# Performance work log

Hardware: AMD Instinct MI355X
Metric: run time of the kernel (lower is better)

The kernel has to match this reference:

```python
import jax, jax.numpy as jnp
import numpy as np

EPS = 1e-10
LEAKY_SLOPE = 0.01


def norm_1(x):
    mx = jnp.max(x)
    mn = jnp.min(x)
    return (x - mn) / (mx - mn + EPS)


def intr(f_cat):
    # channel self-attention: [b,c,h,w] -> attention over channels
    b, c, h, w = f_cat.shape
    fr = f_cat.reshape(b, c, h * w)                      # [b,c,n]
    scores = jnp.einsum('bcn,bdn->bcd', fr, fr)          # [b,c,c]
    W = jax.nn.softmax(scores, axis=1)                   # softmax over dim 1 (rows)
    fw = jnp.einsum('bcd,bdn->bcn', W, fr).reshape(b, c, h, w)
    return norm_1(jnp.maximum(f_cat - jnp.mean(f_cat), EPS)) + fw + f_cat


def conv3x3(x, w, b):
    y = jax.lax.conv_general_dilated(
        x, w, window_strides=(1, 1), padding='SAME',
        dimension_numbers=('NCHW', 'OIHW', 'NCHW'))
    return y + b[None, :, None, None]


def setup_inputs() -> dict:
    key = jax.random.key(0)
    ks = jax.random.split(key, 13)
    shp = (4, 64, 128, 128)
    names = ['E1_0', 'E1_1', 'E2_0', 'E2_1', 'E3_0', 'E3_1', 'E4_0', 'E4_1']
    d = {n: jax.random.normal(k, shp, dtype=jnp.float32)
         for n, k in zip(names, ks[:8])}
    d['fc'] = jax.random.normal(ks[8], (4, 128, 128, 128), dtype=jnp.float32)
    d['conv1_w'] = jax.random.normal(ks[9], (64, 128, 3, 3), dtype=jnp.float32) * 0.05
    d['conv1_b'] = jax.random.normal(ks[10], (64,), dtype=jnp.float32) * 0.05
    d['conv2_w'] = jax.random.normal(ks[11], (1, 64, 3, 3), dtype=jnp.float32) * 0.05
    d['conv2_b'] = jax.random.normal(ks[12], (1,), dtype=jnp.float32) * 0.05
    return d


def reference(E1_0, E1_1, E2_0, E2_1, E3_0, E3_1, E4_0, E4_1, fc,
              conv1_w, conv1_b, conv2_w, conv2_b):
    cat_features = jax.nn.leaky_relu(conv3x3(fc, conv1_w, conv1_b), LEAKY_SLOPE)
    activation_maps = conv3x3(cat_features, conv2_w, conv2_b)
    nam = norm_1(activation_maps)
    Ir_activation = nam
    Vi_activation = 1.0 - nam

    M1 = jnp.concatenate([intr(E1_0), intr(E2_0), intr(E3_0), intr(E4_0)], axis=1)
    M2 = jnp.concatenate([intr(E1_1), intr(E2_1), intr(E3_1), intr(E4_1)], axis=1)

    Ir_map = Ir_activation * cat_features
    Vi_map = Vi_activation * cat_features
    b = E4_0.shape[0]
    return (M1, M2,
            M1.reshape(b, -1), M2.reshape(b, -1),
            Ir_map.reshape(Ir_map.shape[0], -1), Vi_map.reshape(Vi_map.shape[0], -1),
            Ir_activation, Vi_activation)
```

## Files before the change

kernel.cpp:

```cpp
#include <hip/hip_runtime.h>
#include <stdint.h>
#include <math.h>

typedef float f4 __attribute__((ext_vector_type(4)));
typedef float f32x4 __attribute__((ext_vector_type(4)));
typedef short bf16x8 __attribute__((ext_vector_type(8)));
typedef _Float16 f16x8 __attribute__((ext_vector_type(8)));
typedef unsigned short u16;
typedef unsigned short u16x4 __attribute__((ext_vector_type(4)));

#define NPIX 16384

#define O_M1   0l
#define O_M2   16777216l
#define O_M1F  33554432l
#define O_M2F  50331648l
#define O_IR   67108864l
#define O_VI   71303168l
#define O_IRA  75497472l
#define O_VIA  75563008l
#define FLATD  33554432l

#define WS_SUMP 0
#define WS_MMXE 4096
#define WS_MMXA 4160
#define WS_MEAN 4224
#define WS_MNT  4256
#define WS_INV  4288
#define WS_W1M  8192
#define WS_AM   262144
#define WS_WB   524288

struct EPtrs { const float* p[8]; };

__device__ __forceinline__ u16 f2bf(float x){
  unsigned u = __float_as_uint(x);
  unsigned r = (u + 0x7fffu + ((u >> 16) & 1u)) >> 16;
  return (u16)r;
}
__device__ __forceinline__ float bf2f(u16 v){
  return __uint_as_float(((unsigned)v) << 16);
}
__device__ __forceinline__ u16 f2h(float x){
  _Float16 h = (_Float16)x;
  u16 r; __builtin_memcpy(&r, &h, 2);
  return r;
}
__device__ __forceinline__ unsigned fenc(float x){
  unsigned u = __float_as_uint(x);
  return (u & 0x80000000u) ? ~u : (u | 0x80000000u);
}
__device__ __forceinline__ float fdec(unsigned u){
  unsigned v = (u & 0x80000000u) ? (u & 0x7fffffffu) : ~u;
  return __uint_as_float(v);
}

__global__ void k_prep(const float* __restrict__ w1, u16* __restrict__ w1m,
                       unsigned* mmxe, unsigned* mmxa){
  if (blockIdx.x == 0 && threadIdx.x < 9){
    int t = threadIdx.x;
    if (t < 8){ mmxe[2*t] = 0xFFFFFFFFu; mmxe[2*t+1] = 0u; }
    else      { mmxa[0] = 0xFFFFFFFFu; mmxa[1] = 0u; }
  }
  int i = blockIdx.x*256 + threadIdx.x;
  if (i < 73728){
    int ic32 = i & 31;
    int oc   = (i >> 5) & 63;
    int k9   = (i >> 11) % 9;
    int icc  = i / 18432;
    float v = w1[(oc*128 + icc*32 + ic32)*9 + k9];
    w1m[i] = f2h(v);
  }
}

__global__ __launch_bounds__(256) void k_stats_gram(EPtrs eps,
    float* __restrict__ gram, float* __restrict__ sump, unsigned* __restrict__ mmxe){
  int bid = blockIdx.x;
  int t = bid >> 7; int rb = bid & 127; int b = rb >> 5; int s = rb & 31;
  const float* E = eps.p[t];
  __shared__ u16 lds[64*136];
  __shared__ float red[768];
  int tid = threadIdx.x;
  int lane = tid & 63, wave = tid >> 6;
  f32x4 acc[4];
  #pragma unroll
  for (int i=0;i<4;++i) acc[i] = (f32x4){0.f,0.f,0.f,0.f};
  float vmin = 3.4e38f, vmax = -3.4e38f, vsum = 0.f;
  int rowS = tid >> 5;
  int colS = (tid & 31) * 4;
  int rA = wave*16 + (lane & 15);
  int kb = (lane >> 4) * 8;
  long nbase = (long)s * 512;
  for (int ch = 0; ch < 4; ++ch){
    long n0 = nbase + ch*128;
    __syncthreads();
    #pragma unroll
    for (int p = 0; p < 8; ++p){
      int row = p*8 + rowS;
      f4 v = *(const f4*)&E[(long)(b*64 + row)*NPIX + n0 + colS];
      vsum += v[0]+v[1]+v[2]+v[3];
      vmin = fminf(vmin, fminf(fminf(v[0],v[1]), fminf(v[2],v[3])));
      vmax = fmaxf(vmax, fmaxf(fmaxf(v[0],v[1]), fmaxf(v[2],v[3])));
      u16x4 w; w[0]=f2bf(v[0]); w[1]=f2bf(v[1]); w[2]=f2bf(v[2]); w[3]=f2bf(v[3]);
      *(u16x4*)&lds[row*136 + colS] = w;
    }
    __syncthreads();
    #pragma unroll
    for (int ks = 0; ks < 4; ++ks){
      bf16x8 a = *(bf16x8*)&lds[rA*136 + ks*32 + kb];
      #pragma unroll
      for (int cb = 0; cb < 4; ++cb){
        bf16x8 bb = *(bf16x8*)&lds[(cb*16 + (lane&15))*136 + ks*32 + kb];
        acc[cb] = __builtin_amdgcn_mfma_f32_16x16x32_bf16(a, bb, acc[cb], 0, 0, 0);
      }
    }
  }
  long gbase = ((long)((t*4 + b)*32 + s)) * 4096;
  #pragma unroll
  for (int cb = 0; cb < 4; ++cb){
    int d = cb*16 + (lane & 15);
    #pragma unroll
    for (int rr = 0; rr < 4; ++rr){
      int c = 16*wave + 4*(lane>>4) + rr;
      gram[gbase + c*64 + d] = acc[cb][rr];
    }
  }
  red[tid] = vsum; red[256+tid] = vmin; red[512+tid] = vmax;
  __syncthreads();
  for (int off = 128; off > 0; off >>= 1){
    if (tid < off){
      red[tid] += red[tid+off];
      red[256+tid] = fminf(red[256+tid], red[256+tid+off]);
      red[512+tid] = fmaxf(red[512+tid], red[512+tid+off]);
    }
    __syncthreads();
  }
  if (tid == 0){
    sump[t*128 + b*32 + s] = red[0];
    atomicMin(&mmxe[2*t], fenc(red[256]));
    atomicMax(&mmxe[2*t+1], fenc(red[512]));
  }
}

__global__ __launch_bounds__(1024) void k_softmax(const float* __restrict__ gram,
                          u16* __restrict__ Wb,
                          const float* __restrict__ sump, const unsigned* __restrict__ mmxe,
                          float* __restrict__ meanA, float* __restrict__ mntA, float* __restrict__ invA){
  int bid = blockIdx.x; int t = bid >> 2; int b = bid & 3;
  __shared__ float S[64*68];
  int tid = threadIdx.x;
  if (b == 0 && tid == 0){
    float s = 0.f;
    for (int j = 0; j < 128; ++j) s += sump[t*128 + j];
    float mean = s / 4194304.0f;
    float mn = fdec(mmxe[2*t]), mx = fdec(mmxe[2*t+1]);
    float mnt = fmaxf(mn - mean, 1e-10f);
    float mxt = fmaxf(mx - mean, 1e-10f);
    meanA[t] = mean; mntA[t] = mnt;
    invA[t] = 1.0f / (mxt - mnt + 1e-10f);
  }
  long gb = (long)(t*4 + b)*32*4096;
  {
    int i = tid;
    f4 a = (f4){0.f,0.f,0.f,0.f};
    #pragma unroll
    for (int s = 0; s < 32; ++s) a += *(const f4*)&gram[gb + s*4096 + i*4];
    int c = i >> 4, d0 = (i & 15)*4;
    *(f4*)&S[c*68 + d0] = a;
  }
  __syncthreads();
  if (tid < 64){
    int d = tid;
    float mx = -3.4e38f;
    for (int c = 0; c < 64; ++c) mx = fmaxf(mx, S[c*68+d]);
    float sum = 0.f;
    for (int c = 0; c < 64; ++c){ float e = expf(S[c*68+d]-mx); S[c*68+d] = e; sum += e; }
    float inv = 1.0f/sum;
    long wb = (long)(t*4 + b)*4096;
    for (int c = 0; c < 64; ++c) Wb[wb + c*64 + d] = f2bf(S[c*68+d]*inv);
  }
}

__global__ __launch_bounds__(512) void k_conv1(const float* __restrict__ fc,
    const u16* __restrict__ w1m, const float* __restrict__ b1, float* __restrict__ cat){
  int bid = blockIdx.x;
  int vb = (bid & 7)*64 + (bid >> 3);
  int b = vb >> 7, h = vb & 127;
  __shared__ u16 xin[32*3*140];
  int tid = threadIdx.x;
  int lane = tid & 63, wv = tid >> 6;
  int mg = wv >> 2, ng = wv & 3;
  int l15 = lane & 15, lq = lane >> 4;
  if (tid < 192){
    int ic = tid / 6, rem = tid % 6;
    int r = rem >> 1, sx = (rem & 1) ? 132 : 3;
    xin[(ic*3 + r)*140 + sx] = 0;
  }
  f32x4 acc[2][2];
  #pragma unroll
  for (int i=0;i<2;++i)
    #pragma unroll
    for (int j=0;j<2;++j) acc[i][j] = (f32x4){0.f,0.f,0.f,0.f};
  for (int icc = 0; icc < 4; ++icc){
    __syncthreads();
    #pragma unroll
    for (int it = 0; it < 6; ++it){
      int idx = tid + it*512;
      int ic = idx / 96, rem = idx % 96;
      int r = rem >> 5, q = rem & 31;
      int hr = h + r - 1;
      f4 v = (f4){0.f,0.f,0.f,0.f};
      if ((unsigned)hr < 128u)
        v = *(const f4*)&fc[(long)((b*128 + icc*32 + ic)*128 + hr)*128 + 4*q];
      u16x4 w; w[0]=f2h(v[0]); w[1]=f2h(v[1]); w[2]=f2h(v[2]); w[3]=f2h(v[3]);
      *(u16x4*)&xin[(ic*3 + r)*140 + 4 + 4*q] = w;
    }
    __syncthreads();
    #pragma unroll
    for (int kh = 0; kh < 3; ++kh){
      #pragma unroll
      for (int kw = 0; kw < 3; ++kw){
        int k9 = kh*3 + kw;
        f16x8 A[2];
        #pragma unroll
        for (int mi = 0; mi < 2; ++mi){
          int m = mg*2 + mi;
          A[mi] = *(const f16x8*)&w1m[(((icc*9 + k9)*64) + m*16 + l15)*32 + lq*8];
        }
        #pragma unroll
        for (int ji = 0; ji < 2; ++ji){
          int s = ng*32 + ji*16 + l15 + kw + 3;
          int kb = lq*8;
          f16x8 bv;
          #pragma unroll
          for (int e = 0; e < 8; ++e){
            u16 raw = xin[((kb + e)*3 + kh)*140 + s];
            _Float16 hh; __builtin_memcpy(&hh, &raw, 2);
            bv[e] = hh;
          }
          acc[0][ji] = __builtin_amdgcn_mfma_f32_16x16x32_f16(A[0], bv, acc[0][ji], 0, 0, 0);
          acc[1][ji] = __builtin_amdgcn_mfma_f32_16x16x32_f16(A[1], bv, acc[1][ji], 0, 0, 0);
        }
      }
    }
  }
  #pragma unroll
  for (int mi = 0; mi < 2; ++mi){
    #pragma unroll
    for (int rr = 0; rr < 4; ++rr){
      int oc = (mg*2 + mi)*16 + lq*4 + rr;
      float bb = b1[oc];
      #pragma unroll
      for (int ji = 0; ji < 2; ++ji){
        int w = ng*32 + ji*16 + l15;
        float v = acc[mi][ji][rr] + bb;
        v = v > 0.f ? v : 0.01f*v;
        cat[(long)((b*64 + oc)*128 + h)*128 + w] = v;
      }
    }
  }
}

__global__ __launch_bounds__(256) void k_conv2(const float* __restrict__ cat,
    const float* __restrict__ w2, const float* __restrict__ b2p,
    float* __restrict__ am, unsigned* __restrict__ mmxa){
  int bid = blockIdx.x; int b = bid >> 7; int h = bid & 127;
  __shared__ u16 l2[64*3*136];
  __shared__ float w2l[576];
  __shared__ float red2[256];
  int tid = threadIdx.x;
  for (int i = tid; i < 576; i += 256) w2l[i] = w2[i];
  if (tid < 192){
    int ic = tid / 3, r = tid % 3;
    l2[ic*408 + r*136 + 3]   = 0;
    l2[ic*408 + r*136 + 132] = 0;
  }
  #pragma unroll
  for (int rep = 0; rep < 3; ++rep){
    int idx = rep*256 + tid;
    int ic = idx / 12; int rem = idx - ic*12; int r = rem >> 2; int q = rem & 3;
    int hr = h + r - 1;
    #pragma unroll
    for (int k = 0; k < 8; ++k){
      int w = q*32 + 4*k;
      f4 v = (f4){0.f,0.f,0.f,0.f};
      if ((unsigned)hr < 128u)
        v = *(const f4*)&cat[(long)((b*64 + ic)*128 + hr)*128 + w];
      u16x4 u; u[0]=f2bf(v[0]); u[1]=f2bf(v[1]); u[2]=f2bf(v[2]); u[3]=f2bf(v[3]);
      *(u16x4*)&l2[ic*408 + r*136 + 4 + w] = u;
    }
  }
  __syncthreads();
  int w = tid & 127, icg = tid >> 7;
  float a = 0.f;
  for (int ic = icg*32; ic < icg*32+32; ++ic){
    #pragma unroll
    for (int r = 0; r < 3; ++r)
      #pragma unroll
      for (int kw = 0; kw < 3; ++kw)
        a = fmaf(bf2f(l2[ic*408 + r*136 + (w + kw + 3)]), w2l[ic*9 + r*3 + kw], a);
  }
  red2[tid] = a;
  __syncthreads();
  float av = 0.f;
  if (icg == 0){
    av = red2[w] + red2[128 + w] + b2p[0];
    am[(long)(b*128 + h)*128 + w] = av;
  }
  __syncthreads();
  red2[tid] = (icg == 0) ? av : -3.4e38f;
  __syncthreads();
  for (int off = 128; off > 0; off >>= 1){
    if (tid < off) red2[tid] = fmaxf(red2[tid], red2[tid+off]);
    __syncthreads();
  }
  if (tid == 0) atomicMax(&mmxa[1], fenc(red2[0]));
  __syncthreads();
  red2[tid] = (icg == 0) ? av : 3.4e38f;
  __syncthreads();
  for (int off = 128; off > 0; off >>= 1){
    if (tid < off) red2[tid] = fminf(red2[tid], red2[tid+off]);
    __syncthreads();
  }
  if (tid == 0) atomicMin(&mmxa[0], fenc(red2[0]));
}

__global__ void k_maps(const float* __restrict__ am,
                       const unsigned* __restrict__ mmxa, float* __restrict__ out){
  int bid = blockIdx.x;
  int tid = threadIdx.x;
  float mn = fdec(mmxa[0]);
  float inv = 1.0f / (fdec(mmxa[1]) - mn + 1e-10f);
  long e = ((long)bid*256 + tid) * 4;
  f4 c = *(const f4*)&out[O_IR + e];
  f4 a = *(const f4*)&am[(e >> 20)*16384 + (e & 16383)];
  f4 nam = (a - mn) * inv;
  f4 ir = nam * c;
  f4 vi = (1.0f - nam) * c;
  __builtin_nontemporal_store(ir, (f4*)&out[O_IR + e]);
  __builtin_nontemporal_store(vi, (f4*)&out[O_VI + e]);
  if (tid < 4){
    long e2 = ((long)bid*4 + tid) * 4;
    f4 a2 = *(const f4*)&am[e2];
    f4 nam2 = (a2 - mn) * inv;
    f4 via = 1.0f - nam2;
    __builtin_nontemporal_store(nam2, (f4*)&out[O_IRA + e2]);
    __builtin_nontemporal_store(via,  (f4*)&out[O_VIA + e2]);
  }
}

__global__ __launch_bounds__(256, 4) void k_fuse(EPtrs eps, const u16* __restrict__ Wb,
    const float* __restrict__ meanA, const float* __restrict__ mntA, const float* __restrict__ invA,
    float* __restrict__ out){
  int bid = blockIdx.x;
  int t = bid >> 9; int rem = bid & 511; int b = rem >> 7; int nt = rem & 127;
  const float* E = eps.p[t];
  const u16* Wp = Wb + (long)(t*4 + b)*4096;
  __shared__ float tileF[8192];
  int tid = threadIdx.x; int lane = tid & 63; int w = tid >> 6;
  int jc = lane & 15, lq = lane >> 4;
  long n0 = (long)nt * 128;
  long eb = (long)(b*64) * NPIX;
  bf16x8 Wf[2][4];
  #pragma unroll
  for (int ks = 0; ks < 2; ++ks)
    #pragma unroll
    for (int ci = 0; ci < 4; ++ci)
      Wf[ks][ci] = *(const bf16x8*)&Wp[(ci*16 + jc)*64 + ks*32 + lq*8];
  #pragma unroll
  for (int it = 0; it < 8; ++it){
    int a = it*4 + w;
    int c0 = (a >> 1) << 2;
    int n = (a & 1)*64 + lane;
    long src = eb + (long)c0*NPIX + n0 + n;
    float f0 = E[src];
    float f1 = E[src + NPIX];
    float f2 = E[src + 2*NPIX];
    float f3 = E[src + 3*NPIX];
    f32x4 v = {f0, f1, f2, f3};
    *(f32x4*)&tileF[n*64 + (((c0 >> 2) ^ (n & 15)) << 2)] = v;
  }
  __syncthreads();
  f32x4 acc[2][4];
  #pragma unroll
  for (int i=0;i<2;++i)
    #pragma unroll
    for (int j=0;j<4;++j) acc[i][j] = (f32x4){0.f,0.f,0.f,0.f};
  int nw = w*32;
  #pragma unroll
  for (int ks = 0; ks < 2; ++ks){
    #pragma unroll
    for (int j = 0; j < 2; ++j){
      int n_t = nw + j*16 + jc;
      int p = ks*8 + lq*2;
      const float* base = &tileF[n_t*64];
      f32x4 q0 = *(const f32x4*)&base[(p ^ jc) << 2];
      f32x4 q1 = *(const f32x4*)&base[((p+1) ^ jc) << 2];
      bf16x8 av;
      av[0]=(short)f2bf(q0[0]); av[1]=(short)f2bf(q0[1]);
      av[2]=(short)f2bf(q0[2]); av[3]=(short)f2bf(q0[3]);
      av[4]=(short)f2bf(q1[0]); av[5]=(short)f2bf(q1[1]);
      av[6]=(short)f2bf(q1[2]); av[7]=(short)f2bf(q1[3]);
      #pragma unroll
      for (int ci = 0; ci < 4; ++ci)
        acc[j][ci] = __builtin_amdgcn_mfma_f32_16x16x32_bf16(av, Wf[ks][ci], acc[j][ci], 0, 0, 0);
    }
  }
  float mean = meanA[t], mnt = mntA[t], inv = invA[t];
  long Mbase = (t & 1) ? O_M2 : O_M1;
  long gr = t >> 1;
  #pragma unroll
  for (int j = 0; j < 2; ++j){
    int nbase2 = nw + j*16 + lq*4;
    #pragma unroll
    for (int ci = 0; ci < 4; ++ci){
      int c = ci*16 + jc;
      f4 vals;
      #pragma unroll
      for (int rr = 0; rr < 4; ++rr){
        int n_t = nbase2 + rr;
        float f = tileF[n_t*64 + ((((c >> 2) ^ (n_t & 15)) << 2) + (c & 3))];
        float tv = fmaxf(f - mean, 1e-10f);
        vals[rr] = (tv - mnt)*inv + acc[j][ci][rr] + f;
      }
      long dst = Mbase + ((long)(b*256 + gr*64 + c))*NPIX + n0 + nbase2;
      __builtin_nontemporal_store(vals, (f4*)&out[dst]);
      __builtin_nontemporal_store(vals, (f4*)&out[dst + FLATD]);
    }
  }
}

extern "C" void kernel_launch(void* const* d_in, const int* in_sizes, int n_in,
                              void* d_out, int out_size, void* d_ws, size_t ws_size,
                              hipStream_t stream){
  (void)in_sizes; (void)n_in; (void)out_size; (void)ws_size;
  EPtrs ep;
  for (int i = 0; i < 8; ++i) ep.p[i] = (const float*)d_in[i];
  const float* fc = (const float*)d_in[8];
  const float* w1 = (const float*)d_in[9];
  const float* b1 = (const float*)d_in[10];
  const float* w2 = (const float*)d_in[11];
  const float* b2 = (const float*)d_in[12];
  float* out = (float*)d_out;
  char* ws = (char*)d_ws;
  float* sump   = (float*)(ws + WS_SUMP);
  unsigned* mmxe = (unsigned*)(ws + WS_MMXE);
  unsigned* mmxa = (unsigned*)(ws + WS_MMXA);
  float* meanA  = (float*)(ws + WS_MEAN);
  float* mntA   = (float*)(ws + WS_MNT);
  float* invA   = (float*)(ws + WS_INV);
  u16*   w1m    = (u16*)(ws + WS_W1M);
  float* am     = (float*)(ws + WS_AM);
  u16*   Wb     = (u16*)(ws + WS_WB);
  float* gram = out + O_M1F;
  float* cat  = out + O_IR;

  k_prep      <<<288, 256, 0, stream>>>(w1, w1m, mmxe, mmxa);
  k_conv1     <<<512, 512, 0, stream>>>(fc, w1m, b1, cat);
  k_conv2     <<<512, 256, 0, stream>>>(cat, w2, b2, am, mmxa);
  k_maps      <<<4096,256, 0, stream>>>(am, mmxa, out);
  k_stats_gram<<<1024,256, 0, stream>>>(ep, gram, sump, mmxe);
  k_softmax   <<<32, 1024, 0, stream>>>(gram, Wb, sump, mmxe, meanA, mntA, invA);
  k_fuse      <<<4096,256, 0, stream>>>(ep, Wb, meanA, mntA, invA, out);
}
```

Baseline: 201.1 us.

## Merge independent stages into combined kernels to run stats/gram alongside conv

Independent work is packed into shared launches. Stats+gram and conv1 now run in one kernel, dispatched by block index. Conv2 and softmax share a second kernel, which uses a shared-memory union. Conv1 drops from 512 threads to 256 per block, with each wave covering 64 columns instead of 32. The aim is to cut launch gaps and let the memory-bound gram blocks overlap with the compute-bound conv blocks, at the cost of higher register use in conv1 and fewer threads for the softmax gram reduction.

```diff
diff --git a/kernel.cpp b/kernel.cpp
--- a/kernel.cpp
+++ b/kernel.cpp
@@ -73,256 +73,257 @@
   }
 }
 
-__global__ __launch_bounds__(256) void k_stats_gram(EPtrs eps,
-    float* __restrict__ gram, float* __restrict__ sump, unsigned* __restrict__ mmxe){
+struct SGsh { u16 lds[64*136]; float red[768]; };
+struct C1sh { u16 xin[32*3*140]; };
+union  KAsh { SGsh sg; C1sh c1; };
+
+__global__ __launch_bounds__(256) void k_A(EPtrs eps,
+    const float* __restrict__ fc, const u16* __restrict__ w1m, const float* __restrict__ b1,
+    float* __restrict__ gram, float* __restrict__ sump, unsigned* __restrict__ mmxe,
+    float* __restrict__ cat){
+  __shared__ KAsh sh;
   int bid = blockIdx.x;
-  int t = bid >> 7; int rb = bid & 127; int b = rb >> 5; int s = rb & 31;
-  const float* E = eps.p[t];
-  __shared__ u16 lds[64*136];
-  __shared__ float red[768];
   int tid = threadIdx.x;
   int lane = tid & 63, wave = tid >> 6;
-  f32x4 acc[4];
-  #pragma unroll
-  for (int i=0;i<4;++i) acc[i] = (f32x4){0.f,0.f,0.f,0.f};
-  float vmin = 3.4e38f, vmax = -3.4e38f, vsum = 0.f;
-  int rowS = tid >> 5;
-  int colS = (tid & 31) * 4;
-  int rA = wave*16 + (lane & 15);
-  int kb = (lane >> 4) * 8;
-  long nbase = (long)s * 512;
-  for (int ch = 0; ch < 4; ++ch){
-    long n0 = nbase + ch*128;
-    __syncthreads();
-    #pragma unroll
-    for (int p = 0; p < 8; ++p){
-      int row = p*8 + rowS;
-      f4 v = *(const f4*)&E[(long)(b*64 + row)*NPIX + n0 + colS];
-      vsum += v[0]+v[1]+v[2]+v[3];
-      vmin = fminf(vmin, fminf(fminf(v[0],v[1]), fminf(v[2],v[3])));
-      vmax = fmaxf(vmax, fmaxf(fmaxf(v[0],v[1]), fmaxf(v[2],v[3])));
-      u16x4 w; w[0]=f2bf(v[0]); w[1]=f2bf(v[1]); w[2]=f2bf(v[2]); w[3]=f2bf(v[3]);
-      *(u16x4*)&lds[row*136 + colS] = w;
-    }
-    __syncthreads();
-    #pragma unroll
-    for (int ks = 0; ks < 4; ++ks){
-      bf16x8 a = *(bf16x8*)&lds[rA*136 + ks*32 + kb];
-      #pragma unroll
-      for (int cb = 0; cb < 4; ++cb){
-        bf16x8 bb = *(bf16x8*)&lds[(cb*16 + (lane&15))*136 + ks*32 + kb];
-        acc[cb] = __builtin_amdgcn_mfma_f32_16x16x32_bf16(a, bb, acc[cb], 0, 0, 0);
-      }
-    }
-  }
-  long gbase = ((long)((t*4 + b)*32 + s)) * 4096;
-  #pragma unroll
-  for (int cb = 0; cb < 4; ++cb){
-    int d = cb*16 + (lane & 15);
-    #pragma unroll
-    for (int rr = 0; rr < 4; ++rr){
-      int c = 16*wave + 4*(lane>>4) + rr;
-      gram[gbase + c*64 + d] = acc[cb][rr];
-    }
-  }
-  red[tid] = vsum; red[256+tid] = vmin; red[512+tid] = vmax;
-  __syncthreads();
-  for (int off = 128; off > 0; off >>= 1){
-    if (tid < off){
-      red[tid] += red[tid+off];
-      red[256+tid] = fminf(red[256+tid], red[256+tid+off]);
-      red[512+tid] = fmaxf(red[512+tid], red[512+tid+off]);
-    }
-    __syncthreads();
-  }
-  if (tid == 0){
-    sump[t*128 + b*32 + s] = red[0];
-    atomicMin(&mmxe[2*t], fenc(red[256]));
-    atomicMax(&mmxe[2*t+1], fenc(red[512]));
-  }
-}
-
-__global__ __launch_bounds__(1024) void k_softmax(const float* __restrict__ gram,
-                          u16* __restrict__ Wb,
-                          const float* __restrict__ sump, const unsigned* __restrict__ mmxe,
-                          float* __restrict__ meanA, float* __restrict__ mntA, float* __restrict__ invA){
-  int bid = blockIdx.x; int t = bid >> 2; int b = bid & 3;
-  __shared__ float S[64*68];
+  if (bid < 1024){
+    int t = bid >> 7; int rb = bid & 127; int b = rb >> 5; int s = rb & 31;
+    const float* E = eps.p[t];
+    f32x4 acc[4];
+    #pragma unroll
+    for (int i=0;i<4;++i) acc[i] = (f32x4){0.f,0.f,0.f,0.f};
+    float vmin = 3.4e38f, vmax = -3.4e38f, vsum = 0.f;
+    int rowS = tid >> 5;
+    int colS = (tid & 31) * 4;
+    int rA = wave*16 + (lane & 15);
+    int kb = (lane >> 4) * 8;
+    long nbase = (long)s * 512;
+    for (int ch = 0; ch < 4; ++ch){
+      long n0 = nbase + ch*128;
+      __syncthreads();
+      #pragma unroll
+      for (int p = 0; p < 8; ++p){
+        int row = p*8 + rowS;
+        f4 v = *(const f4*)&E[(long)(b*64 + row)*NPIX + n0 + colS];
+        vsum += v[0]+v[1]+v[2]+v[3];
+        vmin = fminf(vmin, fminf(fminf(v[0],v[1]), fminf(v[2],v[3])));
+        vmax = fmaxf(vmax, fmaxf(fmaxf(v[0],v[1]), fmaxf(v[2],v[3])));
+        u16x4 w; w[0]=f2bf(v[0]); w[1]=f2bf(v[1]); w[2]=f2bf(v[2]); w[3]=f2bf(v[3]);
+        *(u16x4*)&sh.sg.lds[row*136 + colS] = w;
+      }
+      __syncthreads();
+      #pragma unroll
+      for (int ks = 0; ks < 4; ++ks){
+        bf16x8 a = *(bf16x8*)&sh.sg.lds[rA*136 + ks*32 + kb];
+        #pragma unroll
+        for (int cb = 0; cb < 4; ++cb){
+          bf16x8 bb = *(bf16x8*)&sh.sg.lds[(cb*16 + (lane&15))*136 + ks*32 + kb];
+          acc[cb] = __builtin_amdgcn_mfma_f32_16x16x32_bf16(a, bb, acc[cb], 0, 0, 0);
+        }
+      }
+    }
+    long gbase = ((long)((t*4 + b)*32 + s)) * 4096;
+    #pragma unroll
+    for (int cb = 0; cb < 4; ++cb){
+      int d = cb*16 + (lane & 15);
+      #pragma unroll
+      for (int rr = 0; rr < 4; ++rr){
+        int c = 16*wave + 4*(lane>>4) + rr;
+        gram[gbase + c*64 + d] = acc[cb][rr];
+      }
+    }
+    sh.sg.red[tid] = vsum; sh.sg.red[256+tid] = vmin; sh.sg.red[512+tid] = vmax;
+    __syncthreads();
+    for (int off = 128; off > 0; off >>= 1){
+      if (tid < off){
+        sh.sg.red[tid] += sh.sg.red[tid+off];
+        sh.sg.red[256+tid] = fminf(sh.sg.red[256+tid], sh.sg.red[256+tid+off]);
+        sh.sg.red[512+tid] = fmaxf(sh.sg.red[512+tid], sh.sg.red[512+tid+off]);
+      }
+      __syncthreads();
+    }
+    if (tid == 0){
+      sump[t*128 + b*32 + s] = sh.sg.red[0];
+      atomicMin(&mmxe[2*t], fenc(sh.sg.red[256]));
+      atomicMax(&mmxe[2*t+1], fenc(sh.sg.red[512]));
+    }
+  } else {
+    int cb = bid - 1024;
+    int vb = (cb & 7)*64 + (cb >> 3);
+    int b = vb >> 7, h = vb & 127;
+    int mg = wave >> 1, ng = wave & 1;
+    int l15 = lane & 15, lq = lane >> 4;
+    if (tid < 192){
+      int ic = tid / 6, rem = tid % 6;
+      int r = rem >> 1, sx = (rem & 1) ? 132 : 3;
+      sh.c1.xin[(ic*3 + r)*140 + sx] = 0;
+    }
+    f32x4 acc[2][4];
+    #pragma unroll
+    for (int i=0;i<2;++i)
+      #pragma unroll
+      for (int j=0;j<4;++j) acc[i][j] = (f32x4){0.f,0.f,0.f,0.f};
+    for (int icc = 0; icc < 4; ++icc){
+      __syncthreads();
+      #pragma unroll
+      for (int it = 0; it < 12; ++it){
+        int idx = it*256 + tid;
+        int ic = idx / 96, rem = idx % 96;
+        int r = rem >> 5, q = rem & 31;
+        int hr = h + r - 1;
+        f4 v = (f4){0.f,0.f,0.f,0.f};
+        if ((unsigned)hr < 128u)
+          v = *(const f4*)&fc[(long)((b*128 + icc*32 + ic)*128 + hr)*128 + 4*q];
+        u16x4 w; w[0]=f2h(v[0]); w[1]=f2h(v[1]); w[2]=f2h(v[2]); w[3]=f2h(v[3]);
+        *(u16x4*)&sh.c1.xin[(ic*3 + r)*140 + 4 + 4*q] = w;
+      }
+      __syncthreads();
+      #pragma unroll
+      for (int kh = 0; kh < 3; ++kh){
+        #pragma unroll
+        for (int kw = 0; kw < 3; ++kw){
+          int k9 = kh*3 + kw;
+          f16x8 A[2];
+          #pragma unroll
+          for (int mi = 0; mi < 2; ++mi){
+            int m = mg*2 + mi;
+            A[mi] = *(const f16x8*)&w1m[(((icc*9 + k9)*64) + m*16 + l15)*32 + lq*8];
+          }
+          #pragma unroll
+          for (int ji = 0; ji < 4; ++ji){
+            int s = ng*64 + ji*16 + l15 + kw + 3;
+            int kb = lq*8;
+            f16x8 bv;
+            #pragma unroll
+            for (int e = 0; e < 8; ++e){
+              u16 raw = sh.c1.xin[((kb + e)*3 + kh)*140 + s];
+              _Float16 hh; __builtin_memcpy(&hh, &raw, 2);
+              bv[e] = hh;
+            }
+            acc[0][ji] = __builtin_amdgcn_mfma_f32_16x16x32_f16(A[0], bv, acc[0][ji], 0, 0, 0);
+            acc[1][ji] = __builtin_amdgcn_mfma_f32_16x16x32_f16(A[1], bv, acc[1][ji], 0, 0, 0);
+          }
+        }
+      }
+    }
+    #pragma unroll
+    for (int mi = 0; mi < 2; ++mi){
+      #pragma unroll
+      for (int rr = 0; rr < 4; ++rr){
+        int oc = (mg*2 + mi)*16 + lq*4 + rr;
+        float bb = b1[oc];
+        #pragma unroll
+        for (int ji = 0; ji < 4; ++ji){
+          int w = ng*64 + ji*16 + l15;
+          float v = acc[mi][ji][rr] + bb;
+          v = v > 0.f ? v : 0.01f*v;
+          cat[(long)((b*64 + oc)*128 + h)*128 + w] = v;
+        }
+      }
+    }
+  }
+}
+
+struct C2sh { u16 l2[64*3*136]; float w2l[576]; float red2[256]; };
+struct SMsh { float S[64*68]; };
+union  KBsh { C2sh c2; SMsh sm; };
+
+__global__ __launch_bounds__(256) void k_B(const float* __restrict__ gram,
+    u16* __restrict__ Wb, const float* __restrict__ sump, const unsigned* __restrict__ mmxe,
+    float* __restrict__ meanA, float* __restrict__ mntA, float* __restrict__ invA,
+    const float* __restrict__ cat, const float* __restrict__ w2, const float* __restrict__ b2p,
+    float* __restrict__ am, unsigned* __restrict__ mmxa){
+  __shared__ KBsh sh;
+  int bid = blockIdx.x;
   int tid = threadIdx.x;
-  if (b == 0 && tid == 0){
-    float s = 0.f;
-    for (int j = 0; j < 128; ++j) s += sump[t*128 + j];
-    float mean = s / 4194304.0f;
-    float mn = fdec(mmxe[2*t]), mx = fdec(mmxe[2*t+1]);
-    float mnt = fmaxf(mn - mean, 1e-10f);
-    float mxt = fmaxf(mx - mean, 1e-10f);
-    meanA[t] = mean; mntA[t] = mnt;
-    invA[t] = 1.0f / (mxt - mnt + 1e-10f);
-  }
-  long gb = (long)(t*4 + b)*32*4096;
-  {
-    int i = tid;
-    f4 a = (f4){0.f,0.f,0.f,0.f};
-    #pragma unroll
-    for (int s = 0; s < 32; ++s) a += *(const f4*)&gram[gb + s*4096 + i*4];
-    int c = i >> 4, d0 = (i & 15)*4;
-    *(f4*)&S[c*68 + d0] = a;
-  }
-  __syncthreads();
-  if (tid < 64){
-    int d = tid;
-    float mx = -3.4e38f;
-    for (int c = 0; c < 64; ++c) mx = fmaxf(mx, S[c*68+d]);
-    float sum = 0.f;
-    for (int c = 0; c < 64; ++c){ float e = expf(S[c*68+d]-mx); S[c*68+d] = e; sum += e; }
-    float inv = 1.0f/sum;
-    long wb = (long)(t*4 + b)*4096;
-    for (int c = 0; c < 64; ++c) Wb[wb + c*64 + d] = f2bf(S[c*68+d]*inv);
-  }
-}
-
-__global__ __launch_bounds__(512) void k_conv1(const float* __restrict__ fc,
-    const u16* __restrict__ w1m, const float* __restrict__ b1, float* __restrict__ cat){
-  int bid = blockIdx.x;
-  int vb = (bid & 7)*64 + (bid >> 3);
-  int b = vb >> 7, h = vb & 127;
-  __shared__ u16 xin[32*3*140];
-  int tid = threadIdx.x;
-  int lane = tid & 63, wv = tid >> 6;
-  int mg = wv >> 2, ng = wv & 3;
-  int l15 = lane & 15, lq = lane >> 4;
-  if (tid < 192){
-    int ic = tid / 6, rem = tid % 6;
-    int r = rem >> 1, sx = (rem & 1) ? 132 : 3;
-    xin[(ic*3 + r)*140 + sx] = 0;
-  }
-  f32x4 acc[2][2];
-  #pragma unroll
-  for (int i=0;i<2;++i)
-    #pragma unroll
-    for (int j=0;j<2;++j) acc[i][j] = (f32x4){0.f,0.f,0.f,0.f};
-  for (int icc = 0; icc < 4; ++icc){
-    __syncthreads();
-    #pragma unroll
-    for (int it = 0; it < 6; ++it){
-      int idx = tid + it*512;
-      int ic = idx / 96, rem = idx % 96;
-      int r = rem >> 5, q = rem & 31;
+  if (bid < 512){
+    int b = bid >> 7; int h = bid & 127;
+    for (int i = tid; i < 576; i += 256) sh.c2.w2l[i] = w2[i];
+    if (tid < 192){
+      int ic = tid / 3, r = tid % 3;
+      sh.c2.l2[ic*408 + r*136 + 3]   = 0;
+      sh.c2.l2[ic*408 + r*136 + 132] = 0;
+    }
+    #pragma unroll
+    for (int rep = 0; rep < 3; ++rep){
+      int idx = rep*256 + tid;
+      int ic = idx / 12; int rem = idx - ic*12; int r = rem >> 2; int q = rem & 3;
       int hr = h + r - 1;
-      f4 v = (f4){0.f,0.f,0.f,0.f};
-      if ((unsigned)hr < 128u)
-        v = *(const f4*)&fc[(long)((b*128 + icc*32 + ic)*128 + hr)*128 + 4*q];
-      u16x4 w; w[0]=f2h(v[0]); w[1]=f2h(v[1]); w[2]=f2h(v[2]); w[3]=f2h(v[3]);
-      *(u16x4*)&xin[(ic*3 + r)*140 + 4 + 4*q] = w;
-    }
-    __syncthreads();
-    #pragma unroll
-    for (int kh = 0; kh < 3; ++kh){
-      #pragma unroll
-      for (int kw = 0; kw < 3; ++kw){
-        int k9 = kh*3 + kw;
-        f16x8 A[2];
+      #pragma unroll
+      for (int k = 0; k < 8; ++k){
+        int w = q*32 + 4*k;
+        f4 v = (f4){0.f,0.f,0.f,0.f};
+        if ((unsigned)hr < 128u)
+          v = *(const f4*)&cat[(long)((b*64 + ic)*128 + hr)*128 + w];
+        u16x4 u; u[0]=f2bf(v[0]); u[1]=f2bf(v[1]); u[2]=f2bf(v[2]); u[3]=f2bf(v[3]);
+        *(u16x4*)&sh.c2.l2[ic*408 + r*136 + 4 + w] = u;
+      }
+    }
+    __syncthreads();
+    int w = tid & 127, icg = tid >> 7;
+    float a = 0.f;
+    for (int ic = icg*32; ic < icg*32+32; ++ic){
+      #pragma unroll
+      for (int r = 0; r < 3; ++r)
         #pragma unroll
-        for (int mi = 0; mi < 2; ++mi){
-          int m = mg*2 + mi;
-          A[mi] = *(const f16x8*)&w1m[(((icc*9 + k9)*64) + m*16 + l15)*32 + lq*8];
-        }
-        #pragma unroll
-        for (int ji = 0; ji < 2; ++ji){
-          int s = ng*32 + ji*16 + l15 + kw + 3;
-          int kb = lq*8;
-          f16x8 bv;
-          #pragma unroll
-          for (int e = 0; e < 8; ++e){
-            u16 raw = xin[((kb + e)*3 + kh)*140 + s];
-            _Float16 hh; __builtin_memcpy(&hh, &raw, 2);
-            bv[e] = hh;
-          }
-          acc[0][ji] = __builtin_amdgcn_mfma_f32_16x16x32_f16(A[0], bv, acc[0][ji], 0, 0, 0);
-          acc[1][ji] = __builtin_amdgcn_mfma_f32_16x16x32_f16(A[1], bv, acc[1][ji], 0, 0, 0);
-        }
-      }
-    }
-  }
-  #pragma unroll
-  for (int mi = 0; mi < 2; ++mi){
-    #pragma unroll
-    for (int rr = 0; rr < 4; ++rr){
-      int oc = (mg*2 + mi)*16 + lq*4 + rr;
-      float bb = b1[oc];
-      #pragma unroll
-      for (int ji = 0; ji < 2; ++ji){
-        int w = ng*32 + ji*16 + l15;
-        float v = acc[mi][ji][rr] + bb;
-        v = v > 0.f ? v : 0.01f*v;
-        cat[(long)((b*64 + oc)*128 + h)*128 + w] = v;
-      }
-    }
-  }
-}
-
-__global__ __launch_bounds__(256) void k_conv2(const float* __restrict__ cat,
-    const float* __restrict__ w2, const float* __restrict__ b2p,
-    float* __restrict__ am, unsigned* __restrict__ mmxa){
-  int bid = blockIdx.x; int b = bid >> 7; int h = bid & 127;
-  __shared__ u16 l2[64*3*136];
-  __shared__ float w2l[576];
-  __shared__ float red2[256];
-  int tid = threadIdx.x;
-  for (int i = tid; i < 576; i += 256) w2l[i] = w2[i];
-  if (tid < 192){
-    int ic = tid / 3, r = tid % 3;
-    l2[ic*408 + r*136 + 3]   = 0;
-    l2[ic*408 + r*136 + 132] = 0;
-  }
-  #pragma unroll
-  for (int rep = 0; rep < 3; ++rep){
-    int idx = rep*256 + tid;
-    int ic = idx / 12; int rem = idx - ic*12; int r = rem >> 2; int q = rem & 3;
-    int hr = h + r - 1;
-    #pragma unroll
-    for (int k = 0; k < 8; ++k){
-      int w = q*32 + 4*k;
-      f4 v = (f4){0.f,0.f,0.f,0.f};
-      if ((unsigned)hr < 128u)
-        v = *(const f4*)&cat[(long)((b*64 + ic)*128 + hr)*128 + w];
-      u16x4 u; u[0]=f2bf(v[0]); u[1]=f2bf(v[1]); u[2]=f2bf(v[2]); u[3]=f2bf(v[3]);
-      *(u16x4*)&l2[ic*408 + r*136 + 4 + w] = u;
-    }
-  }
-  __syncthreads();
-  int w = tid & 127, icg = tid >> 7;
-  float a = 0.f;
-  for (int ic = icg*32; ic < icg*32+32; ++ic){
-    #pragma unroll
-    for (int r = 0; r < 3; ++r)
-      #pragma unroll
-      for (int kw = 0; kw < 3; ++kw)
-        a = fmaf(bf2f(l2[ic*408 + r*136 + (w + kw + 3)]), w2l[ic*9 + r*3 + kw], a);
-  }
-  red2[tid] = a;
-  __syncthreads();
-  float av = 0.f;
-  if (icg == 0){
-    av = red2[w] + red2[128 + w] + b2p[0];
-    am[(long)(b*128 + h)*128 + w] = av;
-  }
-  __syncthreads();
-  red2[tid] = (icg == 0) ? av : -3.4e38f;
-  __syncthreads();
-  for (int off = 128; off > 0; off >>= 1){
-    if (tid < off) red2[tid] = fmaxf(red2[tid], red2[tid+off]);
-    __syncthreads();
-  }
-  if (tid == 0) atomicMax(&mmxa[1], fenc(red2[0]));
-  __syncthreads();
-  red2[tid] = (icg == 0) ? av : 3.4e38f;
-  __syncthreads();
-  for (int off = 128; off > 0; off >>= 1){
-    if (tid < off) red2[tid] = fminf(red2[tid], red2[tid+off]);
-    __syncthreads();
-  }
-  if (tid == 0) atomicMin(&mmxa[0], fenc(red2[0]));
+        for (int kw = 0; kw < 3; ++kw)
+          a = fmaf(bf2f(sh.c2.l2[ic*408 + r*136 + (w + kw + 3)]), sh.c2.w2l[ic*9 + r*3 + kw], a);
+    }
+    sh.c2.red2[tid] = a;
+    __syncthreads();
+    float av = 0.f;
+    if (icg == 0){
+      av = sh.c2.red2[w] + sh.c2.red2[128 + w] + b2p[0];
+      am[(long)(b*128 + h)*128 + w] = av;
+    }
+    __syncthreads();
+    sh.c2.red2[tid] = (icg == 0) ? av : -3.4e38f;
+    __syncthreads();
+    for (int off = 128; off > 0; off >>= 1){
+      if (tid < off) sh.c2.red2[tid] = fmaxf(sh.c2.red2[tid], sh.c2.red2[tid+off]);
+      __syncthreads();
+    }
+    if (tid == 0) atomicMax(&mmxa[1], fenc(sh.c2.red2[0]));
+    __syncthreads();
+    sh.c2.red2[tid] = (icg == 0) ? av : 3.4e38f;
+    __syncthreads();
+    for (int off = 128; off > 0; off >>= 1){
+      if (tid < off) sh.c2.red2[tid] = fminf(sh.c2.red2[tid], sh.c2.red2[tid+off]);
+      __syncthreads();
+    }
+    if (tid == 0) atomicMin(&mmxa[0], fenc(sh.c2.red2[0]));
+  } else {
+    int sb = bid - 512;
+    int t = sb >> 2; int b = sb & 3;
+    if (b == 0 && tid == 0){
+      float s = 0.f;
+      for (int j = 0; j < 128; ++j) s += sump[t*128 + j];
+      float mean = s / 4194304.0f;
+      float mn = fdec(mmxe[2*t]), mx = fdec(mmxe[2*t+1]);
+      float mnt = fmaxf(mn - mean, 1e-10f);
+      float mxt = fmaxf(mx - mean, 1e-10f);
+      meanA[t] = mean; mntA[t] = mnt;
+      invA[t] = 1.0f / (mxt - mnt + 1e-10f);
+    }
+    long gb = (long)(t*4 + b)*32*4096;
+    for (int i = tid; i < 1024; i += 256){
+      f4 a = (f4){0.f,0.f,0.f,0.f};
+      #pragma unroll
+      for (int s = 0; s < 32; ++s) a += *(const f4*)&gram[gb + s*4096 + i*4];
+      int c = i >> 4, d0 = (i & 15)*4;
+      *(f4*)&sh.sm.S[c*68 + d0] = a;
+    }
+    __syncthreads();
+    if (tid < 64){
+      int d = tid;
+      float mx = -3.4e38f;
+      for (int c = 0; c < 64; ++c) mx = fmaxf(mx, sh.sm.S[c*68+d]);
+      float sum = 0.f;
+      for (int c = 0; c < 64; ++c){ float e = expf(sh.sm.S[c*68+d]-mx); sh.sm.S[c*68+d] = e; sum += e; }
+      float inv = 1.0f/sum;
+      long wb = (long)(t*4 + b)*4096;
+      for (int c = 0; c < 64; ++c) Wb[wb + c*64 + d] = f2bf(sh.sm.S[c*68+d]*inv);
+    }
+  }
 }
 
 __global__ void k_maps(const float* __restrict__ am,
@@ -455,11 +456,10 @@
   float* gram = out + O_M1F;
   float* cat  = out + O_IR;
 
-  k_prep      <<<288, 256, 0, stream>>>(w1, w1m, mmxe, mmxa);
-  k_conv1     <<<512, 512, 0, stream>>>(fc, w1m, b1, cat);
-  k_conv2     <<<512, 256, 0, stream>>>(cat, w2, b2, am, mmxa);
-  k_maps      <<<4096,256, 0, stream>>>(am, mmxa, out);
-  k_stats_gram<<<1024,256, 0, stream>>>(ep, gram, sump, mmxe);
-  k_softmax   <<<32, 1024, 0, stream>>>(gram, Wb, sump, mmxe, meanA, mntA, invA);
-  k_fuse      <<<4096,256, 0, stream>>>(ep, Wb, meanA, mntA, invA, out);
-}
+  k_prep <<<288,  256, 0, stream>>>(w1, w1m, mmxe, mmxa);
+  k_A    <<<1536, 256, 0, stream>>>(ep, fc, w1m, b1, gram, sump, mmxe, cat);
+  k_B    <<<544,  256, 0, stream>>>(gram, Wb, sump, mmxe, meanA, mntA, invA,
+                                    cat, w2, b2, am, mmxa);
+  k_maps <<<4096, 256, 0, stream>>>(am, mmxa, out);
+  k_fuse <<<4096, 256, 0, stream>>>(ep, Wb, meanA, mntA, invA, out);
+}
```

Measured after the change: 197.8 us. Within noise of the previous version (-1.6%).
